# Optimization experiments

Measured on AMD Instinct MI355X. Metric: run time of the kernel, lower is better.

## Reference

```python
import jax, jax.numpy as jnp
import numpy as np

N = 50000          # nodes
E = 800000         # edges (avg degree 16)
IN, HID, OUT = 128, 128, 64
LAMBDA_MAX = 2.0   # DGL default convention for scaled Laplacian (re_norm = 2/lambda_max = 1)


def setup_inputs() -> dict:
    key = jax.random.key(0)
    k1, k2, k3, k4, k5 = jax.random.split(key, 5)
    features = jax.random.normal(k1, (N, IN), dtype=jnp.float32)
    src = jax.random.randint(k2, (E,), 0, N)
    dst = jax.random.randint(k3, (E,), 0, N)
    # ChebConv(k=2) linear: Linear(2*in, out), torch default uniform init
    s1 = 1.0 / np.sqrt(2 * IN)
    W1 = jax.random.uniform(k4, (2 * IN, HID), jnp.float32, -s1, s1)
    b1 = jnp.zeros((HID,), jnp.float32)
    s2 = 1.0 / np.sqrt(2 * HID)
    W2 = jax.random.uniform(k5, (2 * HID, OUT), jnp.float32, -s2, s2)
    b2 = jnp.zeros((OUT,), jnp.float32)
    return {"features": features, "src": src, "dst": dst,
            "W1": W1, "b1": b1, "W2": W2, "b2": b2}


def _cheb_conv(x, src, dst, d_invsqrt, W, b, re_norm):
    msg = (x * d_invsqrt)[src]                                   # [E, d]
    h = jax.ops.segment_sum(msg, dst, num_segments=N) * d_invsqrt  # [N, d]
    # X_1 = L_tilde X_0 = -re_norm * A_hat X + (re_norm - 1) * X
    x1 = -re_norm * h + x * (re_norm - 1.0)
    xt = jnp.concatenate([x, x1], axis=1)                        # [N, 2d]
    return xt @ W + b


def reference(features, src, dst, W1, b1, W2, b2):
    deg = jax.ops.segment_sum(jnp.ones((E,), jnp.float32), dst, num_segments=N)
    d_invsqrt = jnp.power(jnp.clip(deg, 1.0, None), -0.5)[:, None]  # [N,1]
    re_norm = 2.0 / LAMBDA_MAX
    h = _cheb_conv(features, src, dst, d_invsqrt, W1, b1, re_norm)
    # dropout omitted (eval mode)
    h = _cheb_conv(h, src, dst, d_invsqrt, W2, b2, re_norm)
    return h
```

## Files before the change

kernel.cpp:

```cpp
#include <hip/hip_runtime.h>

#define IN_DIM  128

typedef __bf16 bf16x8 __attribute__((ext_vector_type(8)));
typedef float  f32x4  __attribute__((ext_vector_type(4)));

static inline size_t align256(size_t x) { return (x + 255) & ~size_t(255); }

__device__ __forceinline__ ushort f2b1(float f) {
    union { float f; uint u; } c; c.f = f;
    uint u = c.u;
    uint r = (u + 0x7FFFu + ((u >> 16) & 1u)) >> 16;
    return (ushort)r;
}
__device__ __forceinline__ float lo_bf(uint v) {
    union { uint u; float f; } c; c.u = v << 16; return c.f;
}
__device__ __forceinline__ float hi_bf(uint v) {
    union { uint u; float f; } c; c.u = v & 0xffff0000u; return c.f;
}


__global__ void zero_kernel(int4* __restrict__ p, int n16) {
    int i = blockIdx.x * blockDim.x + threadIdx.x;
    if (i < n16) p[i] = make_int4(0, 0, 0, 0);
}

__global__ void hist_kernel(const int* __restrict__ dst, int* __restrict__ deg,
                            int* __restrict__ rank, int E) {
    int e = blockIdx.x * blockDim.x + threadIdx.x;
    if (e < E) rank[e] = atomicAdd(&deg[dst[e]], 1);
}

__global__ __launch_bounds__(256) void scan_blocks(const int* __restrict__ deg,
                                                   int* __restrict__ pre,
                                                   int* __restrict__ bsum, int n) {
    __shared__ int sh[256];
    int t = threadIdx.x;
    int base = blockIdx.x * 1024 + t * 4;
    int v0 = 0, v1 = 0, v2 = 0, v3 = 0;
    if (base + 3 < n) {
        int4 v = *reinterpret_cast<const int4*>(deg + base);
        v0 = v.x; v1 = v.y; v2 = v.z; v3 = v.w;
    } else {
        if (base     < n) v0 = deg[base];
        if (base + 1 < n) v1 = deg[base + 1];
        if (base + 2 < n) v2 = deg[base + 2];
        if (base + 3 < n) v3 = deg[base + 3];
    }
    int s = v0 + v1 + v2 + v3;
    sh[t] = s;
    __syncthreads();
    for (int off = 1; off < 256; off <<= 1) {
        int x = (t >= off) ? sh[t - off] : 0;
        __syncthreads();
        sh[t] += x;
        __syncthreads();
    }
    int excl = sh[t] - s;
    if (t == 255) bsum[blockIdx.x] = sh[255];
    if (base     < n) pre[base]     = excl;
    if (base + 1 < n) pre[base + 1] = excl + v0;
    if (base + 2 < n) pre[base + 2] = excl + v0 + v1;
    if (base + 3 < n) pre[base + 3] = excl + v0 + v1 + v2;
}


template <typename CT>
__global__ __launch_bounds__(256) void phase2_kernel(
    const int* __restrict__ src, const int* __restrict__ dst,
    const int* __restrict__ pre, const int* __restrict__ bsum,
    const int* __restrict__ deg, const int* __restrict__ rank,
    CT* __restrict__ col, int E, int fillBlocks,
    const float* __restrict__ feats,
    ushort* __restrict__ featbs, ushort* __restrict__ z2s, int N, int nbF, int nb,
    const float* __restrict__ W1, ushort* __restrict__ W1t,
    const float* __restrict__ W2, ushort* __restrict__ W2ct)
{
    __shared__ int sb[64];
    int b = blockIdx.x, t = threadIdx.x;
    if (t < 64) {
        int orig = (t < nb) ? bsum[t] : 0;
        int v = orig;
        for (int off = 1; off < 64; off <<= 1) {
            int u = __shfl_up(v, off);
            if (t >= off) v += u;
        }
        sb[t] = v - orig;
    }
    __syncthreads();

    if (b < fillBlocks) {
        int e0 = (b * 256 + t) * 4;
        if (e0 + 3 < E) {
            int4 d4 = *reinterpret_cast<const int4*>(dst + e0);
            int4 r4 = *reinterpret_cast<const int4*>(rank + e0);
            int4 s4 = *reinterpret_cast<const int4*>(src + e0);
            col[pre[d4.x] + sb[d4.x >> 10] + r4.x] = (CT)s4.x;
            col[pre[d4.y] + sb[d4.y >> 10] + r4.y] = (CT)s4.y;
            col[pre[d4.z] + sb[d4.z >> 10] + r4.z] = (CT)s4.z;
            col[pre[d4.w] + sb[d4.w >> 10] + r4.w] = (CT)s4.w;
        } else {
            for (int e = e0; e < E; ++e) {
                int d = dst[e];
                col[pre[d] + sb[d >> 10] + rank[e]] = (CT)src[e];
            }
        }
        return;
    }
    int b2 = b - fillBlocks;
    if (b2 < nbF) {
        size_t i4 = (size_t)b2 * 256 + t;
        if (i4 < (size_t)N * 32) {
            size_t i = i4 * 4;
            float4 v = *reinterpret_cast<const float4*>(feats + i);
            int node = (int)(i4 >> 5);
            int d = deg[node]; if (d < 1) d = 1;
            float dv = rsqrtf((float)d);
            ushort4 os;
            os.x = f2b1(v.x * dv); os.y = f2b1(v.y * dv); os.z = f2b1(v.z * dv); os.w = f2b1(v.w * dv);
            *reinterpret_cast<ushort4*>(featbs + i) = os;
        }
    } else if (b2 < nbF + 128) {
        if (b2 == nbF) {
            if (t < 32) *reinterpret_cast<uint2*>(featbs + (size_t)N * 128 + t * 4) = make_uint2(0, 0);
            else if (t < 48) *reinterpret_cast<uint2*>(z2s + (size_t)N * 64 + (t - 32) * 4) = make_uint2(0, 0);
        }
        int i = (b2 - nbF) * 256 + t;
        int k = i >> 7, c = i & 127;
        W1t[(size_t)c * 256 + k] = f2b1(W1[i]);
    } else {
        int i = (b2 - nbF - 128) * 256 + t;
        int c = i >> 7, k = i & 127;
        float v = (c < 64) ? W2[(size_t)k * 64 + c]
                           : W2[(size_t)(128 + k) * 64 + (c - 64)];
        W2ct[(size_t)c * 128 + k] = f2b1(v);
    }
}


template <typename CT>
__global__ __launch_bounds__(256) void agg_sum128(
    const ushort* __restrict__ Xs, const int* __restrict__ pre,
    const int* __restrict__ bsum, const int* __restrict__ deg,
    const CT* __restrict__ col,
    ushort* __restrict__ X1, int nNodes, int E, int nb)
{
    int w    = (blockIdx.x * blockDim.x + threadIdx.x) >> 6;
    int lane = threadIdx.x & 63;
    int n0 = w * 2;
    if (n0 >= nNodes) return;
    n0 = __builtin_amdgcn_readfirstlane(n0);

    int orig = (lane < nb) ? bsum[lane] : 0;
    int sv = orig;
    for (int off = 1; off < 64; off <<= 1) {
        int u = __shfl_up(sv, off);
        if (lane >= off) sv += u;
    }
    int sbex = sv - orig;

    bool has1 = (n0 + 1) < nNodes;
    int e0a = pre[n0] + __shfl(sbex, n0 >> 10);
    int e1a = (n0 + 1 == nNodes) ? E : pre[n0 + 1] + __shfl(sbex, (n0 + 1) >> 10);
    int e1b = has1 ? ((n0 + 2 == nNodes) ? E : pre[n0 + 2] + __shfl(sbex, (n0 + 2) >> 10)) : e1a;

    int d0 = deg[n0]; if (d0 < 1) d0 = 1;
    int d1 = has1 ? deg[n0 + 1] : 1; if (d1 < 1) d1 = 1;
    float sca = -rsqrtf((float)d0);
    float scb = -rsqrtf((float)d1);
    const uint* Xu = reinterpret_cast<const uint*>(Xs);

    float a0 = 0.f, a1 = 0.f, b0 = 0.f, b1 = 0.f;
    int basea = e0a, baseb = e1a;
    while (basea < e1a || baseb < e1b) {
        int half = lane >> 5, sl = lane & 31;
        int idx = half ? (baseb + sl) : (basea + sl);
        int ee  = half ? e1b : e1a;
        bool okl = idx < ee;
        int cvl = (int)col[okl ? idx : 0];
        int cv  = okl ? cvl : nNodes;
        int cnta = e1a - basea, cntb = e1b - baseb;
        {
            uint va[16], vb[16];
            #pragma unroll
            for (int j = 0; j < 16; ++j) {
                int s0 = __builtin_amdgcn_readlane(cv, j);
                int s1 = __builtin_amdgcn_readlane(cv, 32 + j);
                va[j] = Xu[(uint)(s0 * 64 + lane)];
                vb[j] = Xu[(uint)(s1 * 64 + lane)];
            }
            #pragma unroll
            for (int j = 0; j < 16; ++j) {
                a0 += lo_bf(va[j]); a1 += hi_bf(va[j]);
                b0 += lo_bf(vb[j]); b1 += hi_bf(vb[j]);
            }
        }
        if (cnta > 16 || cntb > 16) {
            uint va[16], vb[16];
            #pragma unroll
            for (int j = 0; j < 16; ++j) {
                int s0 = __builtin_amdgcn_readlane(cv, 16 + j);
                int s1 = __builtin_amdgcn_readlane(cv, 48 + j);
                va[j] = Xu[(uint)(s0 * 64 + lane)];
                vb[j] = Xu[(uint)(s1 * 64 + lane)];
            }
            #pragma unroll
            for (int j = 0; j < 16; ++j) {
                a0 += lo_bf(va[j]); a1 += hi_bf(va[j]);
                b0 += lo_bf(vb[j]); b1 += hi_bf(vb[j]);
            }
        }
        basea += 32; baseb += 32;
    }
    uint oA = (uint)f2b1(a0 * sca) | ((uint)f2b1(a1 * sca) << 16);
    reinterpret_cast<uint*>(X1)[(uint)(n0 * 64 + lane)] = oA;
    if (has1) {
        uint oB = (uint)f2b1(b0 * scb) | ((uint)f2b1(b1 * scb) << 16);
        reinterpret_cast<uint*>(X1)[(uint)((n0 + 1) * 64 + lane)] = oB;
    }
}


template <typename CT>
__global__ __launch_bounds__(256) void agg_sum64(
    const ushort* __restrict__ Zs, const int* __restrict__ pre,
    const int* __restrict__ bsum, const int* __restrict__ deg,
    const CT* __restrict__ col,
    float* __restrict__ Y, int nNodes, int E, int nb)
{
    int w    = (blockIdx.x * blockDim.x + threadIdx.x) >> 6;
    int lane = threadIdx.x & 63;
    int n0 = w * 2;
    if (n0 >= nNodes) return;
    n0 = __builtin_amdgcn_readfirstlane(n0);

    int orig = (lane < nb) ? bsum[lane] : 0;
    int sv = orig;
    for (int off = 1; off < 64; off <<= 1) {
        int u = __shfl_up(sv, off);
        if (lane >= off) sv += u;
    }
    int sbex = sv - orig;

    bool has1 = (n0 + 1) < nNodes;
    int e0a = pre[n0] + __shfl(sbex, n0 >> 10);
    int e1a = (n0 + 1 == nNodes) ? E : pre[n0 + 1] + __shfl(sbex, (n0 + 1) >> 10);
    int e1b = has1 ? ((n0 + 2 == nNodes) ? E : pre[n0 + 2] + __shfl(sbex, (n0 + 2) >> 10)) : e1a;

    int d0 = deg[n0]; if (d0 < 1) d0 = 1;
    int d1 = has1 ? deg[n0 + 1] : 1; if (d1 < 1) d1 = 1;
    float sca = -rsqrtf((float)d0);
    float scb = -rsqrtf((float)d1);

    float fa = 0.f, fb = 0.f;
    int basea = e0a, baseb = e1a;
    while (basea < e1a || baseb < e1b) {
        int half = lane >> 5, sl = lane & 31;
        int idx = half ? (baseb + sl) : (basea + sl);
        int ee  = half ? e1b : e1a;
        bool okl = idx < ee;
        int cvl = (int)col[okl ? idx : 0];
        int cv  = okl ? cvl : nNodes;
        int cnta = e1a - basea, cntb = e1b - baseb;
        {
            ushort va[16], vb[16];
            #pragma unroll
            for (int j = 0; j < 16; ++j) {
                int s0 = __builtin_amdgcn_readlane(cv, j);
                int s1 = __builtin_amdgcn_readlane(cv, 32 + j);
                va[j] = Zs[(uint)(s0 * 64 + lane)];
                vb[j] = Zs[(uint)(s1 * 64 + lane)];
            }
            #pragma unroll
            for (int j = 0; j < 16; ++j) {
                fa += lo_bf((uint)va[j]);
                fb += lo_bf((uint)vb[j]);
            }
        }
        if (cnta > 16 || cntb > 16) {
            ushort va[16], vb[16];
            #pragma unroll
            for (int j = 0; j < 16; ++j) {
                int s0 = __builtin_amdgcn_readlane(cv, 16 + j);
                int s1 = __builtin_amdgcn_readlane(cv, 48 + j);
                va[j] = Zs[(uint)(s0 * 64 + lane)];
                vb[j] = Zs[(uint)(s1 * 64 + lane)];
            }
            #pragma unroll
            for (int j = 0; j < 16; ++j) {
                fa += lo_bf((uint)va[j]);
                fb += lo_bf((uint)vb[j]);
            }
        }
        basea += 32; baseb += 32;
    }
    Y[(uint)(n0 * 64 + lane)] += fa * sca;
    if (has1)
        Y[(uint)((n0 + 1) * 64 + lane)] += fb * scb;
}


__global__ __launch_bounds__(256) void gemm_mfma1(
    const ushort* __restrict__ XS, const ushort* __restrict__ XB,
    const ushort* __restrict__ Wt, const float* __restrict__ bias,
    const int* __restrict__ deg, ushort* __restrict__ Y, int nNodes)
{
    __shared__ ushort wlds[128 * 256];
    int t = threadIdx.x;

    #pragma unroll
    for (int it = 0; it < 16; ++it) {
        int i = it * 256 + t;
        int c = i >> 5;
        int o = (i & 31) << 4;
        bf16x8 v = *reinterpret_cast<const bf16x8*>(Wt + ((size_t)c << 8) + (o >> 1));
        *reinterpret_cast<bf16x8*>((char*)wlds + ((size_t)c << 9) + (o ^ ((c & 7) << 4))) = v;
    }
    __syncthreads();

    int wave = t >> 6, lane = t & 63;
    int r16 = lane & 15, g = lane >> 4;
    int nodeBase = blockIdx.x * 128 + wave * 32;

    int arow0 = nodeBase + r16;       if (arow0 > nNodes - 1) arow0 = nNodes - 1;
    int arow1 = nodeBase + 16 + r16;  if (arow1 > nNodes - 1) arow1 = nNodes - 1;
    const ushort* pA0 = XS + (size_t)arow0 * 128;
    const ushort* pA1 = XS + (size_t)arow1 * 128;
    const ushort* pB0 = XB + (size_t)arow0 * 128;
    const ushort* pB1 = XB + (size_t)arow1 * 128;

    f32x4 acc0A[4], acc0B[4], acc1A[4], acc1B[4];
    f32x4 a0A[8], a0B[8], a1A[8], a1B[8];
    #pragma unroll
    for (int i = 0; i < 8; ++i) {
        a0A[i] = f32x4{0,0,0,0}; a0B[i] = f32x4{0,0,0,0};
        a1A[i] = f32x4{0,0,0,0}; a1B[i] = f32x4{0,0,0,0};
    }
    (void)acc0A; (void)acc0B; (void)acc1A; (void)acc1B;

    #pragma unroll
    for (int kb = 0; kb < 8; ++kb) {
        int kk = (kb & 3) * 32 + g * 8;
        bf16x8 v0 = *reinterpret_cast<const bf16x8*>(((kb < 4) ? pA0 : pB0) + kk);
        bf16x8 v1 = *reinterpret_cast<const bf16x8*>(((kb < 4) ? pA1 : pB1) + kk);
        int o = kb * 64 + g * 16;
        #pragma unroll
        for (int ct = 0; ct < 8; ++ct) {
            int c = ct * 16 + r16;
            bf16x8 bfrag = *reinterpret_cast<const bf16x8*>(
                (const char*)wlds + ((size_t)c << 9) + (o ^ ((c & 7) << 4)));
            if (kb < 4) {
                a0A[ct] = __builtin_amdgcn_mfma_f32_16x16x32_bf16(v0, bfrag, a0A[ct], 0, 0, 0);
                a1A[ct] = __builtin_amdgcn_mfma_f32_16x16x32_bf16(v1, bfrag, a1A[ct], 0, 0, 0);
            } else {
                a0B[ct] = __builtin_amdgcn_mfma_f32_16x16x32_bf16(v0, bfrag, a0B[ct], 0, 0, 0);
                a1B[ct] = __builtin_amdgcn_mfma_f32_16x16x32_bf16(v1, bfrag, a1B[ct], 0, 0, 0);
            }
        }
    }

    float sq0[4], sq1[4];
    #pragma unroll
    for (int r = 0; r < 4; ++r) {
        int o0 = nodeBase + g * 4 + r;      if (o0 > nNodes - 1) o0 = nNodes - 1;
        int o1 = nodeBase + 16 + g * 4 + r; if (o1 > nNodes - 1) o1 = nNodes - 1;
        int d0 = deg[o0]; if (d0 < 1) d0 = 1;
        int d1 = deg[o1]; if (d1 < 1) d1 = 1;
        sq0[r] = sqrtf((float)d0);
        sq1[r] = sqrtf((float)d1);
    }

    #pragma unroll
    for (int ct = 0; ct < 8; ++ct) {
        float bv = bias[ct * 16 + r16];
        #pragma unroll
        for (int r = 0; r < 4; ++r) {
            int orow0 = nodeBase + g * 4 + r;
            int orow1 = orow0 + 16;
            if (orow0 < nNodes) Y[(size_t)orow0 * 128 + ct * 16 + r16] = f2b1(a0A[ct][r] * sq0[r] + a0B[ct][r] + bv);
            if (orow1 < nNodes) Y[(size_t)orow1 * 128 + ct * 16 + r16] = f2b1(a1A[ct][r] * sq1[r] + a1B[ct][r] + bv);
        }
    }
}


__global__ __launch_bounds__(256) void gemm_mfma2(
    const ushort* __restrict__ H1, const ushort* __restrict__ W2ct,
    const float* __restrict__ bias, const int* __restrict__ deg,
    float* __restrict__ Yout, ushort* __restrict__ Z2, int nNodes)
{
    __shared__ ushort wlds[128 * 128];
    int t = threadIdx.x;

    #pragma unroll
    for (int it = 0; it < 8; ++it) {
        int i = it * 256 + t;
        int c = i >> 4;
        int o = (i & 15) << 4;
        bf16x8 v = *reinterpret_cast<const bf16x8*>(W2ct + ((size_t)c << 7) + (o >> 1));
        *reinterpret_cast<bf16x8*>((char*)wlds + ((size_t)c << 8) + (o ^ ((c & 7) << 4))) = v;
    }
    __syncthreads();

    int wave = t >> 6, lane = t & 63;
    int r16 = lane & 15, g = lane >> 4;
    int nodeBase = blockIdx.x * 128 + wave * 32;

    int arow0 = nodeBase + r16;       if (arow0 > nNodes - 1) arow0 = nNodes - 1;
    int arow1 = nodeBase + 16 + r16;  if (arow1 > nNodes - 1) arow1 = nNodes - 1;
    const ushort* p0 = H1 + (size_t)arow0 * 128;
    const ushort* p1 = H1 + (size_t)arow1 * 128;

    f32x4 acc0[8], acc1[8];
    #pragma unroll
    for (int i = 0; i < 8; ++i) { acc0[i] = f32x4{0,0,0,0}; acc1[i] = f32x4{0,0,0,0}; }

    #pragma unroll
    for (int kb = 0; kb < 4; ++kb) {
        int kk = kb * 32 + g * 8;
        bf16x8 v0 = *reinterpret_cast<const bf16x8*>(p0 + kk);
        bf16x8 v1 = *reinterpret_cast<const bf16x8*>(p1 + kk);
        int o = kb * 64 + g * 16;
        #pragma unroll
        for (int ct = 0; ct < 8; ++ct) {
            int c = ct * 16 + r16;
            bf16x8 bfrag = *reinterpret_cast<const bf16x8*>(
                (const char*)wlds + ((size_t)c << 8) + (o ^ ((c & 7) << 4)));
            acc0[ct] = __builtin_amdgcn_mfma_f32_16x16x32_bf16(v0, bfrag, acc0[ct], 0, 0, 0);
            acc1[ct] = __builtin_amdgcn_mfma_f32_16x16x32_bf16(v1, bfrag, acc1[ct], 0, 0, 0);
        }
    }

    float dv0[4], dv1[4];
    #pragma unroll
    for (int r = 0; r < 4; ++r) {
        int o0 = nodeBase + g * 4 + r;      if (o0 > nNodes - 1) o0 = nNodes - 1;
        int o1 = nodeBase + 16 + g * 4 + r; if (o1 > nNodes - 1) o1 = nNodes - 1;
        int d0 = deg[o0]; if (d0 < 1) d0 = 1;
        int d1 = deg[o1]; if (d1 < 1) d1 = 1;
        dv0[r] = rsqrtf((float)d0);
        dv1[r] = rsqrtf((float)d1);
    }

    #pragma unroll
    for (int ct = 0; ct < 8; ++ct) {
        float bv = (ct < 4) ? bias[ct * 16 + r16] : 0.f;
        #pragma unroll
        for (int r = 0; r < 4; ++r) {
            int orow0 = nodeBase + g * 4 + r;
            int orow1 = orow0 + 16;
            if (ct < 4) {
                if (orow0 < nNodes) Yout[(size_t)orow0 * 64 + ct * 16 + r16] = acc0[ct][r] + bv;
                if (orow1 < nNodes) Yout[(size_t)orow1 * 64 + ct * 16 + r16] = acc1[ct][r] + bv;
            } else {
                if (orow0 < nNodes) Z2[(size_t)orow0 * 64 + (ct - 4) * 16 + r16] = f2b1(acc0[ct][r] * dv0[r]);
                if (orow1 < nNodes) Z2[(size_t)orow1 * 64 + (ct - 4) * 16 + r16] = f2b1(acc1[ct][r] * dv1[r]);
            }
        }
    }
}


extern "C" void kernel_launch(void* const* d_in, const int* in_sizes, int n_in,
                              void* d_out, int out_size, void* d_ws, size_t ws_size,
                              hipStream_t stream)
{
    const float* feats = (const float*)d_in[0];
    const int*   src   = (const int*)d_in[1];
    const int*   dst   = (const int*)d_in[2];
    const float* W1    = (const float*)d_in[3];
    const float* b1    = (const float*)d_in[4];
    const float* W2    = (const float*)d_in[5];
    const float* b2    = (const float*)d_in[6];
    float* out = (float*)d_out;

    const int N = in_sizes[0] / IN_DIM;
    const int E = in_sizes[1];
    const int NB = (N + 1023) / 1024;

    char* ws = (char*)d_ws;
    size_t off = 0;
    int*    deg    = (int*)(ws + off);    off = align256(off + (size_t)N * 4);
    int*    pre    = (int*)(ws + off);    off = align256(off + (size_t)N * 4);
    int*    bsum   = (int*)(ws + off);    off = align256(off + (size_t)64 * 4);
    int*    rank   = (int*)(ws + off);    off = align256(off + (size_t)E * 4);
    void*   colv   = (void*)(ws + off);   off = align256(off + (size_t)E * 4);
    ushort* featbs = (ushort*)(ws + off); off = align256(off + (size_t)(N + 1) * 128 * 2);
    ushort* x1b    = (ushort*)(ws + off); off = align256(off + (size_t)N * 128 * 2);
    ushort* h1b    = (ushort*)(ws + off); off = align256(off + (size_t)N * 128 * 2);
    ushort* z2s    = (ushort*)(ws + off); off = align256(off + (size_t)(N + 1) * 64 * 2);
    ushort* W1t    = (ushort*)(ws + off); off = align256(off + (size_t)256 * 128 * 2);
    ushort* W2ct   = (ushort*)(ws + off); off = align256(off + (size_t)128 * 128 * 2);

    const bool small = (N <= 65535);

    const int n16 = (N + 3) / 4;
    zero_kernel<<<(n16 + 255) / 256, 256, 0, stream>>>((int4*)deg, n16);
    hist_kernel<<<(E + 255) / 256, 256, 0, stream>>>(dst, deg, rank, E);
    scan_blocks<<<NB, 256, 0, stream>>>(deg, pre, bsum, N);

    const int fillBlocks = ((E + 3) / 4 + 255) / 256;
    const int nbF = (N * 32 + 255) / 256;
    const int p2Blocks = fillBlocks + nbF + 128 + 64;
    if (small)
        phase2_kernel<ushort><<<p2Blocks, 256, 0, stream>>>(
            src, dst, pre, bsum, deg, rank, (ushort*)colv, E, fillBlocks,
            feats, featbs, z2s, N, nbF, NB, W1, W1t, W2, W2ct);
    else
        phase2_kernel<uint><<<p2Blocks, 256, 0, stream>>>(
            src, dst, pre, bsum, deg, rank, (uint*)colv, E, fillBlocks,
            feats, featbs, z2s, N, nbF, NB, W1, W1t, W2, W2ct);

    const int nPairWaves = (N + 1) / 2;
    const int aggBlocks = (nPairWaves * 64 + 255) / 256;
    const int gemmBlocks = (N + 127) / 128;

    if (small)
        agg_sum128<ushort><<<aggBlocks, 256, 0, stream>>>(featbs, pre, bsum, deg, (const ushort*)colv, x1b, N, E, NB);
    else
        agg_sum128<uint><<<aggBlocks, 256, 0, stream>>>(featbs, pre, bsum, deg, (const uint*)colv, x1b, N, E, NB);
    gemm_mfma1<<<gemmBlocks, 256, 0, stream>>>(featbs, x1b, W1t, b1, deg, h1b, N);

    gemm_mfma2<<<gemmBlocks, 256, 0, stream>>>(h1b, W2ct, b2, deg, out, z2s, N);
    if (small)
        agg_sum64<ushort><<<aggBlocks, 256, 0, stream>>>(z2s, pre, bsum, deg, (const ushort*)colv, out, N, E, NB);
    else
        agg_sum64<uint><<<aggBlocks, 256, 0, stream>>>(z2s, pre, bsum, deg, (const uint*)colv, out, N, E, NB);
}
```

Baseline: 145.7 us.

## Convert features to bf16 during histogram pass and use unscaled copy in GEMM1

The fp32-to-bf16 feature conversion and the weight transposes move into the histogram kernel, so they overlap with the atomic degree counting. Phase2 now rescales the bf16 copy by deg^-1/2 instead of reading fp32 features. GEMM1 reads the unscaled bf16 features directly, which removes the per-row sqrt(deg) rescaling and halves the accumulator sets. This costs an extra N×128 bf16 buffer plus one more read and write of it, and the scaled features are now rounded to bf16 twice.

```diff
diff --git a/kernel.cpp b/kernel.cpp
--- a/kernel.cpp
+++ b/kernel.cpp
@@ -19,6 +19,9 @@
 __device__ __forceinline__ float hi_bf(uint v) {
     union { uint u; float f; } c; c.u = v & 0xffff0000u; return c.f;
 }
+__device__ __forceinline__ float b2f(ushort v) {
+    union { uint u; float f; } c; c.u = (uint)v << 16; return c.f;
+}
 
 
 __global__ void zero_kernel(int4* __restrict__ p, int n16) {
@@ -26,11 +29,43 @@
     if (i < n16) p[i] = make_int4(0, 0, 0, 0);
 }
 
-__global__ void hist_kernel(const int* __restrict__ dst, int* __restrict__ deg,
-                            int* __restrict__ rank, int E) {
-    int e = blockIdx.x * blockDim.x + threadIdx.x;
-    if (e < E) rank[e] = atomicAdd(&deg[dst[e]], 1);
-}
+
+__global__ __launch_bounds__(256) void hist_conv(
+    const int* __restrict__ dst, int* __restrict__ deg, int* __restrict__ rank,
+    int E, int histBlocks,
+    const float* __restrict__ feats, ushort* __restrict__ featb, int N, int nbF,
+    const float* __restrict__ W1, ushort* __restrict__ W1t,
+    const float* __restrict__ W2, ushort* __restrict__ W2ct)
+{
+    int b = blockIdx.x, t = threadIdx.x;
+    if (b < histBlocks) {
+        int e = b * 256 + t;
+        if (e < E) rank[e] = atomicAdd(&deg[dst[e]], 1);
+        return;
+    }
+    int b2 = b - histBlocks;
+    if (b2 < nbF) {
+        size_t i4 = (size_t)b2 * 256 + t;
+        if (i4 < (size_t)N * 32) {
+            size_t i = i4 * 4;
+            float4 v = *reinterpret_cast<const float4*>(feats + i);
+            ushort4 o;
+            o.x = f2b1(v.x); o.y = f2b1(v.y); o.z = f2b1(v.z); o.w = f2b1(v.w);
+            *reinterpret_cast<ushort4*>(featb + i) = o;
+        }
+    } else if (b2 < nbF + 128) {
+        int i = (b2 - nbF) * 256 + t;
+        int k = i >> 7, c = i & 127;
+        W1t[(size_t)c * 256 + k] = f2b1(W1[i]);
+    } else {
+        int i = (b2 - nbF - 128) * 256 + t;
+        int c = i >> 7, k = i & 127;
+        float v = (c < 64) ? W2[(size_t)k * 64 + c]
+                           : W2[(size_t)(128 + k) * 64 + (c - 64)];
+        W2ct[(size_t)c * 128 + k] = f2b1(v);
+    }
+}
+
 
 __global__ __launch_bounds__(256) void scan_blocks(const int* __restrict__ deg,
                                                    int* __restrict__ pre,
@@ -72,10 +107,8 @@
     const int* __restrict__ pre, const int* __restrict__ bsum,
     const int* __restrict__ deg, const int* __restrict__ rank,
     CT* __restrict__ col, int E, int fillBlocks,
-    const float* __restrict__ feats,
-    ushort* __restrict__ featbs, ushort* __restrict__ z2s, int N, int nbF, int nb,
-    const float* __restrict__ W1, ushort* __restrict__ W1t,
-    const float* __restrict__ W2, ushort* __restrict__ W2ct)
+    const ushort* __restrict__ featb, ushort* __restrict__ featbs,
+    ushort* __restrict__ z2s, int N, int nbF, int nb)
 {
     __shared__ int sb[64];
     int b = blockIdx.x, t = threadIdx.x;
@@ -113,28 +146,18 @@
         size_t i4 = (size_t)b2 * 256 + t;
         if (i4 < (size_t)N * 32) {
             size_t i = i4 * 4;
-            float4 v = *reinterpret_cast<const float4*>(feats + i);
+            ushort4 v = *reinterpret_cast<const ushort4*>(featb + i);
             int node = (int)(i4 >> 5);
             int d = deg[node]; if (d < 1) d = 1;
             float dv = rsqrtf((float)d);
             ushort4 os;
-            os.x = f2b1(v.x * dv); os.y = f2b1(v.y * dv); os.z = f2b1(v.z * dv); os.w = f2b1(v.w * dv);
+            os.x = f2b1(b2f(v.x) * dv); os.y = f2b1(b2f(v.y) * dv);
+            os.z = f2b1(b2f(v.z) * dv); os.w = f2b1(b2f(v.w) * dv);
             *reinterpret_cast<ushort4*>(featbs + i) = os;
         }
-    } else if (b2 < nbF + 128) {
-        if (b2 == nbF) {
-            if (t < 32) *reinterpret_cast<uint2*>(featbs + (size_t)N * 128 + t * 4) = make_uint2(0, 0);
-            else if (t < 48) *reinterpret_cast<uint2*>(z2s + (size_t)N * 64 + (t - 32) * 4) = make_uint2(0, 0);
-        }
-        int i = (b2 - nbF) * 256 + t;
-        int k = i >> 7, c = i & 127;
-        W1t[(size_t)c * 256 + k] = f2b1(W1[i]);
     } else {
-        int i = (b2 - nbF - 128) * 256 + t;
-        int c = i >> 7, k = i & 127;
-        float v = (c < 64) ? W2[(size_t)k * 64 + c]
-                           : W2[(size_t)(128 + k) * 64 + (c - 64)];
-        W2ct[(size_t)c * 128 + k] = f2b1(v);
+        if (t < 32) *reinterpret_cast<uint2*>(featbs + (size_t)N * 128 + t * 4) = make_uint2(0, 0);
+        else if (t < 48) *reinterpret_cast<uint2*>(z2s + (size_t)N * 64 + (t - 32) * 4) = make_uint2(0, 0);
     }
 }
 
@@ -302,9 +325,9 @@
 
 
 __global__ __launch_bounds__(256) void gemm_mfma1(
-    const ushort* __restrict__ XS, const ushort* __restrict__ XB,
+    const ushort* __restrict__ XA, const ushort* __restrict__ XB,
     const ushort* __restrict__ Wt, const float* __restrict__ bias,
-    const int* __restrict__ deg, ushort* __restrict__ Y, int nNodes)
+    ushort* __restrict__ Y, int nNodes)
 {
     __shared__ ushort wlds[128 * 256];
     int t = threadIdx.x;
@@ -325,50 +348,29 @@
 
     int arow0 = nodeBase + r16;       if (arow0 > nNodes - 1) arow0 = nNodes - 1;
     int arow1 = nodeBase + 16 + r16;  if (arow1 > nNodes - 1) arow1 = nNodes - 1;
-    const ushort* pA0 = XS + (size_t)arow0 * 128;
-    const ushort* pA1 = XS + (size_t)arow1 * 128;
+    const ushort* pA0 = XA + (size_t)arow0 * 128;
+    const ushort* pA1 = XA + (size_t)arow1 * 128;
     const ushort* pB0 = XB + (size_t)arow0 * 128;
     const ushort* pB1 = XB + (size_t)arow1 * 128;
 
-    f32x4 acc0A[4], acc0B[4], acc1A[4], acc1B[4];
-    f32x4 a0A[8], a0B[8], a1A[8], a1B[8];
-    #pragma unroll
-    for (int i = 0; i < 8; ++i) {
-        a0A[i] = f32x4{0,0,0,0}; a0B[i] = f32x4{0,0,0,0};
-        a1A[i] = f32x4{0,0,0,0}; a1B[i] = f32x4{0,0,0,0};
-    }
-    (void)acc0A; (void)acc0B; (void)acc1A; (void)acc1B;
+    f32x4 acc0[8], acc1[8];
+    #pragma unroll
+    for (int i = 0; i < 8; ++i) { acc0[i] = f32x4{0,0,0,0}; acc1[i] = f32x4{0,0,0,0}; }
 
     #pragma unroll
     for (int kb = 0; kb < 8; ++kb) {
         int kk = (kb & 3) * 32 + g * 8;
-        bf16x8 v0 = *reinterpret_cast<const bf16x8*>(((kb < 4) ? pA0 : pB0) + kk);
-        bf16x8 v1 = *reinterpret_cast<const bf16x8*>(((kb < 4) ? pA1 : pB1) + kk);
+        bf16x8 a0 = *reinterpret_cast<const bf16x8*>(((kb < 4) ? pA0 : pB0) + kk);
+        bf16x8 a1 = *reinterpret_cast<const bf16x8*>(((kb < 4) ? pA1 : pB1) + kk);
         int o = kb * 64 + g * 16;
         #pragma unroll
         for (int ct = 0; ct < 8; ++ct) {
             int c = ct * 16 + r16;
             bf16x8 bfrag = *reinterpret_cast<const bf16x8*>(
                 (const char*)wlds + ((size_t)c << 9) + (o ^ ((c & 7) << 4)));
-            if (kb < 4) {
-                a0A[ct] = __builtin_amdgcn_mfma_f32_16x16x32_bf16(v0, bfrag, a0A[ct], 0, 0, 0);
-                a1A[ct] = __builtin_amdgcn_mfma_f32_16x16x32_bf16(v1, bfrag, a1A[ct], 0, 0, 0);
-            } else {
-                a0B[ct] = __builtin_amdgcn_mfma_f32_16x16x32_bf16(v0, bfrag, a0B[ct], 0, 0, 0);
-                a1B[ct] = __builtin_amdgcn_mfma_f32_16x16x32_bf16(v1, bfrag, a1B[ct], 0, 0, 0);
-            }
-        }
-    }
-
-    float sq0[4], sq1[4];
-    #pragma unroll
-    for (int r = 0; r < 4; ++r) {
-        int o0 = nodeBase + g * 4 + r;      if (o0 > nNodes - 1) o0 = nNodes - 1;
-        int o1 = nodeBase + 16 + g * 4 + r; if (o1 > nNodes - 1) o1 = nNodes - 1;
-        int d0 = deg[o0]; if (d0 < 1) d0 = 1;
-        int d1 = deg[o1]; if (d1 < 1) d1 = 1;
-        sq0[r] = sqrtf((float)d0);
-        sq1[r] = sqrtf((float)d1);
+            acc0[ct] = __builtin_amdgcn_mfma_f32_16x16x32_bf16(a0, bfrag, acc0[ct], 0, 0, 0);
+            acc1[ct] = __builtin_amdgcn_mfma_f32_16x16x32_bf16(a1, bfrag, acc1[ct], 0, 0, 0);
+        }
     }
 
     #pragma unroll
@@ -378,8 +380,8 @@
         for (int r = 0; r < 4; ++r) {
             int orow0 = nodeBase + g * 4 + r;
             int orow1 = orow0 + 16;
-            if (orow0 < nNodes) Y[(size_t)orow0 * 128 + ct * 16 + r16] = f2b1(a0A[ct][r] * sq0[r] + a0B[ct][r] + bv);
-            if (orow1 < nNodes) Y[(size_t)orow1 * 128 + ct * 16 + r16] = f2b1(a1A[ct][r] * sq1[r] + a1B[ct][r] + bv);
+            if (orow0 < nNodes) Y[(size_t)orow0 * 128 + ct * 16 + r16] = f2b1(acc0[ct][r] + bv);
+            if (orow1 < nNodes) Y[(size_t)orow1 * 128 + ct * 16 + r16] = f2b1(acc1[ct][r] + bv);
         }
     }
 }
@@ -486,6 +488,7 @@
     int*    bsum   = (int*)(ws + off);    off = align256(off + (size_t)64 * 4);
     int*    rank   = (int*)(ws + off);    off = align256(off + (size_t)E * 4);
     void*   colv   = (void*)(ws + off);   off = align256(off + (size_t)E * 4);
+    ushort* featb  = (ushort*)(ws + off); off = align256(off + (size_t)N * 128 * 2);
     ushort* featbs = (ushort*)(ws + off); off = align256(off + (size_t)(N + 1) * 128 * 2);
     ushort* x1b    = (ushort*)(ws + off); off = align256(off + (size_t)N * 128 * 2);
     ushort* h1b    = (ushort*)(ws + off); off = align256(off + (size_t)N * 128 * 2);
@@ -494,23 +497,26 @@
     ushort* W2ct   = (ushort*)(ws + off); off = align256(off + (size_t)128 * 128 * 2);
 
     const bool small = (N <= 65535);
+    const int nbF = (N * 32 + 255) / 256;
 
     const int n16 = (N + 3) / 4;
     zero_kernel<<<(n16 + 255) / 256, 256, 0, stream>>>((int4*)deg, n16);
-    hist_kernel<<<(E + 255) / 256, 256, 0, stream>>>(dst, deg, rank, E);
+
+    const int histBlocks = (E + 255) / 256;
+    hist_conv<<<histBlocks + nbF + 128 + 64, 256, 0, stream>>>(
+        dst, deg, rank, E, histBlocks, feats, featb, N, nbF, W1, W1t, W2, W2ct);
+
     scan_blocks<<<NB, 256, 0, stream>>>(deg, pre, bsum, N);
 
     const int fillBlocks = ((E + 3) / 4 + 255) / 256;
-    const int nbF = (N * 32 + 255) / 256;
-    const int p2Blocks = fillBlocks + nbF + 128 + 64;
     if (small)
-        phase2_kernel<ushort><<<p2Blocks, 256, 0, stream>>>(
+        phase2_kernel<ushort><<<fillBlocks + nbF + 1, 256, 0, stream>>>(
             src, dst, pre, bsum, deg, rank, (ushort*)colv, E, fillBlocks,
-            feats, featbs, z2s, N, nbF, NB, W1, W1t, W2, W2ct);
+            featb, featbs, z2s, N, nbF, NB);
     else
-        phase2_kernel<uint><<<p2Blocks, 256, 0, stream>>>(
+        phase2_kernel<uint><<<fillBlocks + nbF + 1, 256, 0, stream>>>(
             src, dst, pre, bsum, deg, rank, (uint*)colv, E, fillBlocks,
-            feats, featbs, z2s, N, nbF, NB, W1, W1t, W2, W2ct);
+            featb, featbs, z2s, N, nbF, NB);
 
     const int nPairWaves = (N + 1) / 2;
     const int aggBlocks = (nPairWaves * 64 + 255) / 256;
@@ -520,7 +526,7 @@
         agg_sum128<ushort><<<aggBlocks, 256, 0, stream>>>(featbs, pre, bsum, deg, (const ushort*)colv, x1b, N, E, NB);
     else
         agg_sum128<uint><<<aggBlocks, 256, 0, stream>>>(featbs, pre, bsum, deg, (const uint*)colv, x1b, N, E, NB);
-    gemm_mfma1<<<gemmBlocks, 256, 0, stream>>>(featbs, x1b, W1t, b1, deg, h1b, N);
+    gemm_mfma1<<<gemmBlocks, 256, 0, stream>>>(featb, x1b, W1t, b1, h1b, N);
 
     gemm_mfma2<<<gemmBlocks, 256, 0, stream>>>(h1b, W2ct, b2, deg, out, z2s, N);
     if (small)
```

After: 148.0 us. No clear change (+1.6%).
